# Kernel tuning notes

Hardware: AMD Instinct MI355X
Metric: run time of the kernel (lower is better)

## Reference

```python
import jax, jax.numpy as jnp
import numpy as np

N_AGENTS = 32
STATE_DIM = 6 * N_AGENTS      # 192
CONTROL_DIM = 3 * N_AGENTS    # 96
HIDDEN = 100
NEWTON_ITERS = 40

# Index maps from the cvxpy objective:
#   p[u_x_r]^T u[u_idx] + p[u_y_r]^T u[2*u_idx] + p[u_z_r]^T u[3*u_idx]
_u_idx = np.arange(N_AGENTS)
P_IDX = np.concatenate([3 * np.arange(1, N_AGENTS + 1),
                        4 * np.arange(1, N_AGENTS + 1),
                        5 * np.arange(1, N_AGENTS + 1)])
U_IDX = np.concatenate([_u_idx, 2 * _u_idx, 3 * _u_idx])


def _p_net(t, z, W1, b1, W2, b2, W3, b3):
    # DefaultPNet: MLP on concat([t, z]) with tanh hiddens (hidden_dim=100)
    x = jnp.concatenate([t, z], axis=-1)          # [B, 1+STATE_DIM]
    h = jnp.tanh(x @ W1 + b1)
    h = jnp.tanh(h @ W2 + b2)
    return h @ W3 + b3                            # [B, STATE_DIM]


def _solve_qp(q):
    # min_u q^T u + 0.5||u||^2 + 0.25||u||^4  (unconstrained, strictly convex)
    # Stationarity: q + (1+||u||^2) u = 0 => u = -q/(1+s), s = ||u||^2
    # => s (1+s)^2 = ||q||^2 ; solve scalar cubic per row via Newton.
    r = jnp.sum(q * q, axis=-1)                   # [B]
    s0 = jnp.cbrt(r)                              # good init: s ~ r^(1/3) for large r

    def step(s, _):
        one = 1.0 + s
        f = s * one * one - r
        fp = one * one + 2.0 * s * one
        return jnp.maximum(s - f / fp, 0.0), None

    s, _ = jax.lax.scan(step, s0, None, length=NEWTON_ITERS)
    return -q / (1.0 + s)[:, None]                # [B, CONTROL_DIM]


def setup_inputs() -> dict:
    key = jax.random.key(0)
    ks = jax.random.split(key, 8)
    B = 131072
    in_dim = 1 + STATE_DIM
    sc1 = 1.0 / np.sqrt(in_dim)
    sc2 = 1.0 / np.sqrt(HIDDEN)
    return {
        "z": jax.random.normal(ks[0], (B, STATE_DIM), jnp.float32),
        "t": jax.random.uniform(ks[1], (B, 1), jnp.float32),
        "W1": jax.random.normal(ks[2], (in_dim, HIDDEN), jnp.float32) * sc1,
        "b1": jnp.zeros((HIDDEN,), jnp.float32),
        "W2": jax.random.normal(ks[3], (HIDDEN, HIDDEN), jnp.float32) * sc2,
        "b2": jnp.zeros((HIDDEN,), jnp.float32),
        "W3": jax.random.normal(ks[4], (HIDDEN, STATE_DIM), jnp.float32) * sc2,
        "b3": jnp.zeros((STATE_DIM,), jnp.float32),
    }


def reference(z, t, W1, b1, W2, b2, W3, b3):
    p = _p_net(t, z, W1, b1, W2, b2, W3, b3)      # [B, STATE_DIM]
    # Accumulate linear coefficients onto u (indices overlap, so scatter-add)
    q = jnp.zeros((p.shape[0], CONTROL_DIM), p.dtype).at[:, U_IDX].add(p[:, P_IDX])
    return _solve_qp(q)                            # ustar [B, CONTROL_DIM]
```

## Files before the change

### kernel.cpp

```cpp
#include <hip/hip_runtime.h>


typedef __attribute__((ext_vector_type(8))) short short8;
typedef __attribute__((ext_vector_type(4))) float f32x4;

__device__ __forceinline__ unsigned short f2bf(float f) {
  unsigned u = __float_as_uint(f);
  u += 0x7fffu + ((u >> 16) & 1u);
  return (unsigned short)(u >> 16);
}
__device__ __forceinline__ float bf2f(unsigned short b) {
  return __uint_as_float(((unsigned)b) << 16);
}
__device__ __forceinline__ float tanh_fast(float x) {
  float ax = fabsf(x);
  float e = __builtin_amdgcn_exp2f(ax * -2.88539008177792681f);
  float r = (1.f - e) * __builtin_amdgcn_rcpf(1.f + e);
  return copysignf(r, x);
}

__global__ void cvx_prep(const float* __restrict__ W1, const float* __restrict__ b1,
                         const float* __restrict__ W2, const float* __restrict__ b2,
                         const float* __restrict__ W3, const float* __restrict__ b3,
                         short* __restrict__ pw) {
  int idx = blockIdx.x * 256 + threadIdx.x;

  if (idx < 25088) {
    int kt = idx / 3584, rem = idx % 3584;
    int nt = rem / 512, e = rem % 512;
    int lane = e >> 3, j = e & 7;
    int k = kt * 32 + (lane >> 4) * 8 + j;
    int n = nt * 16 + (lane & 15);
    float wv = 0.f;
    if (n < 100) {
      if (k < 192) wv = W1[(k + 1) * 100 + n];
      else if (k == 192) wv = W1[n];
    }
    unsigned short hi = f2bf(wv);
    unsigned short lo = f2bf(wv - bf2f(hi));
    pw[(kt * 14 + nt * 2) * 512 + e] = (short)hi;
    pw[(kt * 14 + nt * 2 + 1) * 512 + e] = (short)lo;
    return;
  }
  idx -= 25088;
  if (idx < 14336) {
    int kt = idx / 3584, rem = idx % 3584;
    int nt = rem / 512, e = rem % 512;
    int lane = e >> 3, j = e & 7;
    int k = kt * 32 + (lane >> 4) * 8 + j;
    int n = nt * 16 + (lane & 15);
    float wv = (k < 100 && n < 100) ? W2[k * 100 + n] : 0.f;
    unsigned short hi = f2bf(wv);
    unsigned short lo = f2bf(wv - bf2f(hi));
    pw[50176 + (kt * 14 + nt * 2) * 512 + e] = (short)hi;
    pw[50176 + (kt * 14 + nt * 2 + 1) * 512 + e] = (short)lo;
    return;
  }
  idx -= 14336;
  if (idx < 12288) {
    int kt = idx / 3072, rem = idx % 3072;
    int nt = rem / 512, e = rem % 512;
    int lane = e >> 3, j = e & 7;
    int k = kt * 32 + (lane >> 4) * 8 + j;
    int u = nt * 16 + (lane & 15);
    float wv = 0.f;
    if (k < 100) {
      const float* wr = W3 + k * 192;
      if (u <= 31) wv += wr[3 * u + 3];
      if ((u & 1) == 0 && u <= 62) wv += wr[2 * u + 4];
      if (u % 3 == 0 && u <= 93) wv += wr[(5 * u) / 3 + 5];
    }
    unsigned short hi = f2bf(wv);
    unsigned short lo = f2bf(wv - bf2f(hi));
    pw[78848 + (kt * 12 + nt * 2) * 512 + e] = (short)hi;
    pw[78848 + (kt * 12 + nt * 2 + 1) * 512 + e] = (short)lo;
    return;
  }
  idx -= 12288;
  float* pb = (float*)(pw + 103424);
  if (idx < 112) { pb[idx] = (idx < 100) ? b1[idx] : 0.f; return; }
  idx -= 112;
  if (idx < 112) { pb[112 + idx] = (idx < 100) ? b2[idx] : 0.f; return; }
  idx -= 112;
  if (idx < 96) {
    int u = idx;
    float v = 0.f;
    if (u <= 31) v += b3[3 * u + 3];
    if ((u & 1) == 0 && u <= 62) v += b3[2 * u + 4];
    if (u % 3 == 0 && u <= 93) v += b3[(5 * u) / 3 + 5];
    pb[224 + u] = v;
  }
}

__global__ __launch_bounds__(256, 2) void cvx_main(
    const float* __restrict__ zin, const float* __restrict__ tin,
    const short* __restrict__ pw, float* __restrict__ out) {
  __shared__ __align__(16) short wbuf[2][7168];
  __shared__ __align__(16) short hbuf[128 * 136];

  const int tid = threadIdx.x;
  const int wid = tid >> 6;
  const int lane = tid & 63;
  const int l15 = lane & 15;
  const int qd = lane >> 4;
  const int rb = blockIdx.x * 128 + wid * 32;
  const int lrb = wid * 32;

  const short* PW1 = pw;
  const short* PW2 = pw + 50176;
  const short* PW3 = pw + 78848;
  const float* pb1 = (const float*)(pw + 103424);
  const float* pb2 = pb1 + 112;
  const float* pbq = pb1 + 224;

  auto stage = [&](const short* src, int nf, int buf) {
    for (int f = wid; f < nf; f += 4) {
      const short* g = src + f * 512 + lane * 8;
      __builtin_amdgcn_global_load_lds(
          (const __attribute__((address_space(1))) void*)g,
          (__attribute__((address_space(3))) void*)&wbuf[buf][f * 512],
          16, 0, 0);
    }
  };
  stage(PW1, 14, 0);

  {
    int row = lrb + (lane >> 1);
    short8 zz = {0, 0, 0, 0, 0, 0, 0, 0};
    *(short8*)&hbuf[row * 136 + 112 + (lane & 1) * 8] = zz;
  }

  short8 XA[2][7];
#pragma unroll
  for (int mt = 0; mt < 2; mt++) {
    const int row = rb + mt * 16 + l15;
    const float* zr = zin + (size_t)row * 192;
#pragma unroll
    for (int kt = 0; kt < 6; kt++) {
      const f32x4* p0 = (const f32x4*)(zr + kt * 32 + qd * 8);
      f32x4 v0 = p0[0], v1 = p0[1];
      short8 a;
      a[0] = (short)f2bf(v0[0]); a[1] = (short)f2bf(v0[1]);
      a[2] = (short)f2bf(v0[2]); a[3] = (short)f2bf(v0[3]);
      a[4] = (short)f2bf(v1[0]); a[5] = (short)f2bf(v1[1]);
      a[6] = (short)f2bf(v1[2]); a[7] = (short)f2bf(v1[3]);
      XA[mt][kt] = a;
    }
    short8 a7 = {0, 0, 0, 0, 0, 0, 0, 0};
    if (qd == 0) a7[0] = (short)f2bf(tin[row]);
    XA[mt][6] = a7;
  }

  f32x4 acc[2][7];
#pragma unroll
  for (int nt = 0; nt < 7; nt++) {
    float bv = pb1[nt * 16 + l15];
    f32x4 bvv = {bv, bv, bv, bv};
    acc[0][nt] = bvv; acc[1][nt] = bvv;
  }
#pragma unroll
  for (int kt = 0; kt < 7; kt++) {
    __syncthreads();
    if (kt < 6) stage(PW1 + (kt + 1) * 7168, 14, (kt + 1) & 1);
    else        stage(PW2, 14, 1);
    const short* wb = wbuf[kt & 1];
#pragma unroll
    for (int nt = 0; nt < 7; nt++) {
      short8 bhi = *(const short8*)(wb + nt * 1024 + lane * 8);
      short8 blo = *(const short8*)(wb + nt * 1024 + 512 + lane * 8);
#pragma unroll
      for (int mt = 0; mt < 2; mt++) {
        acc[mt][nt] = __builtin_amdgcn_mfma_f32_16x16x32_bf16(XA[mt][kt], bhi, acc[mt][nt], 0, 0, 0);
        acc[mt][nt] = __builtin_amdgcn_mfma_f32_16x16x32_bf16(XA[mt][kt], blo, acc[mt][nt], 0, 0, 0);
      }
    }
  }
#pragma unroll
  for (int mt = 0; mt < 2; mt++)
#pragma unroll
    for (int nt = 0; nt < 7; nt++)
#pragma unroll
      for (int r = 0; r < 4; r++) {
        int row = lrb + mt * 16 + qd * 4 + r;
        hbuf[row * 136 + nt * 16 + l15] = (short)f2bf(tanh_fast(acc[mt][nt][r]));
      }

  short8 HA[2][4];
#pragma unroll
  for (int mt = 0; mt < 2; mt++) {
    int row = lrb + mt * 16 + l15;
#pragma unroll
    for (int kt = 0; kt < 4; kt++)
      HA[mt][kt] = *(const short8*)&hbuf[row * 136 + kt * 32 + qd * 8];
  }
#pragma unroll
  for (int nt = 0; nt < 7; nt++) {
    float bv = pb2[nt * 16 + l15];
    f32x4 bvv = {bv, bv, bv, bv};
    acc[0][nt] = bvv; acc[1][nt] = bvv;
  }
#pragma unroll
  for (int kt = 0; kt < 4; kt++) {
    __syncthreads();
    if (kt < 3) stage(PW2 + (kt + 1) * 7168, 14, (8 + kt) & 1);
    else        stage(PW3, 12, 1);
    const short* wb = wbuf[(7 + kt) & 1];
#pragma unroll
    for (int nt = 0; nt < 7; nt++) {
      short8 bhi = *(const short8*)(wb + nt * 1024 + lane * 8);
      short8 blo = *(const short8*)(wb + nt * 1024 + 512 + lane * 8);
#pragma unroll
      for (int mt = 0; mt < 2; mt++) {
        acc[mt][nt] = __builtin_amdgcn_mfma_f32_16x16x32_bf16(HA[mt][kt], bhi, acc[mt][nt], 0, 0, 0);
        acc[mt][nt] = __builtin_amdgcn_mfma_f32_16x16x32_bf16(HA[mt][kt], blo, acc[mt][nt], 0, 0, 0);
      }
    }
  }
#pragma unroll
  for (int mt = 0; mt < 2; mt++)
#pragma unroll
    for (int nt = 0; nt < 7; nt++)
#pragma unroll
      for (int r = 0; r < 4; r++) {
        int row = lrb + mt * 16 + qd * 4 + r;
        hbuf[row * 136 + nt * 16 + l15] = (short)f2bf(tanh_fast(acc[mt][nt][r]));
      }

#pragma unroll
  for (int mt = 0; mt < 2; mt++) {
    int row = lrb + mt * 16 + l15;
#pragma unroll
    for (int kt = 0; kt < 4; kt++)
      HA[mt][kt] = *(const short8*)&hbuf[row * 136 + kt * 32 + qd * 8];
  }
  f32x4 qacc[2][6];
#pragma unroll
  for (int nt = 0; nt < 6; nt++) {
    float bv = pbq[nt * 16 + l15];
    f32x4 bvv = {bv, bv, bv, bv};
    qacc[0][nt] = bvv; qacc[1][nt] = bvv;
  }
#pragma unroll
  for (int kt = 0; kt < 4; kt++) {
    __syncthreads();
    if (kt < 3) stage(PW3 + (kt + 1) * 6144, 12, (12 + kt) & 1);
    const short* wb = wbuf[(11 + kt) & 1];
#pragma unroll
    for (int nt = 0; nt < 6; nt++) {
      short8 bhi = *(const short8*)(wb + nt * 1024 + lane * 8);
      short8 blo = *(const short8*)(wb + nt * 1024 + 512 + lane * 8);
#pragma unroll
      for (int mt = 0; mt < 2; mt++) {
        qacc[mt][nt] = __builtin_amdgcn_mfma_f32_16x16x32_bf16(HA[mt][kt], bhi, qacc[mt][nt], 0, 0, 0);
        qacc[mt][nt] = __builtin_amdgcn_mfma_f32_16x16x32_bf16(HA[mt][kt], blo, qacc[mt][nt], 0, 0, 0);
      }
    }
  }

#pragma unroll
  for (int mt = 0; mt < 2; mt++) {
    f32x4 rs = {0.f, 0.f, 0.f, 0.f};
#pragma unroll
    for (int nt = 0; nt < 6; nt++) rs += qacc[mt][nt] * qacc[mt][nt];
    float rv[4];
#pragma unroll
    for (int r = 0; r < 4; r++) {
      float v = rs[r];
      v += __shfl_xor(v, 1);
      v += __shfl_xor(v, 2);
      v += __shfl_xor(v, 4);
      v += __shfl_xor(v, 8);
      rv[r] = v;
    }
    float r2 = rv[l15 & 3];
    float s = __builtin_amdgcn_exp2f(__builtin_amdgcn_logf(r2) * 0.333333333333f);
#pragma unroll
    for (int it = 0; it < 8; it++) {
      float one = 1.f + s;
      float fv = fmaf(s * one, one, -r2);
      float fp = one * fmaf(2.f, s, one);
      s = fmaxf(s - fv * __builtin_amdgcn_rcpf(fp), 0.f);
    }
    float myinv = -__builtin_amdgcn_rcpf(1.f + s);
#pragma unroll
    for (int r = 0; r < 4; r++) {
      float inv = __shfl(myinv, (lane & 48) | r);
      int row = rb + mt * 16 + qd * 4 + r;
      float* orow = out + (size_t)row * 96;
#pragma unroll
      for (int nt = 0; nt < 6; nt++)
        orow[nt * 16 + l15] = qacc[mt][nt][r] * inv;
    }
  }
}

extern "C" void kernel_launch(void* const* d_in, const int* in_sizes, int n_in,
                              void* d_out, int out_size, void* d_ws, size_t ws_size,
                              hipStream_t stream) {
  const float* z  = (const float*)d_in[0];
  const float* t  = (const float*)d_in[1];
  const float* W1 = (const float*)d_in[2];
  const float* b1 = (const float*)d_in[3];
  const float* W2 = (const float*)d_in[4];
  const float* b2 = (const float*)d_in[5];
  const float* W3 = (const float*)d_in[6];
  const float* b3 = (const float*)d_in[7];
  float* out = (float*)d_out;
  int B = in_sizes[0] / 192;

  short* pw = (short*)d_ws;
  cvx_prep<<<204, 256, 0, stream>>>(W1, b1, W2, b2, W3, b3, pw);
  cvx_main<<<B / 128, 256, 0, stream>>>(z, t, pw, out);
}
```

Baseline: 205.6 us.

## Drop split-bf16 weights, keep all weights resident in LDS, prefetch next rows

Weights are now stored as a single bf16 copy instead of a hi/lo pair, which halves the MFMA count and weight bytes. All three layers' weights are loaded into LDS once per 512-thread block, replacing the double-buffered per-k-tile staging and its syncs. Each block processes two 256-row chunks, with the second chunk's z loads issued early. The t input is handled as an fp32 rank-1 FMA rather than an extra K tile, and biases are added in the epilogue. The cost is lower precision in the weights and higher LDS and register use per block.

```diff
diff --git a/kernel.cpp b/kernel.cpp
--- a/kernel.cpp
+++ b/kernel.cpp
@@ -1,16 +1,17 @@
 #include <hip/hip_runtime.h>
+#include <hip/hip_bf16.h>
 
 
 typedef __attribute__((ext_vector_type(8))) short short8;
+typedef __attribute__((ext_vector_type(4))) short short4v;
 typedef __attribute__((ext_vector_type(4))) float f32x4;
+
+#define HST 116
 
 __device__ __forceinline__ unsigned short f2bf(float f) {
   unsigned u = __float_as_uint(f);
   u += 0x7fffu + ((u >> 16) & 1u);
   return (unsigned short)(u >> 16);
-}
-__device__ __forceinline__ float bf2f(unsigned short b) {
-  return __uint_as_float(((unsigned)b) << 16);
 }
 __device__ __forceinline__ float tanh_fast(float x) {
   float ax = fabsf(x);
@@ -25,24 +26,17 @@
                          short* __restrict__ pw) {
   int idx = blockIdx.x * 256 + threadIdx.x;
 
-  if (idx < 25088) {
+  if (idx < 21504) {
     int kt = idx / 3584, rem = idx % 3584;
     int nt = rem / 512, e = rem % 512;
     int lane = e >> 3, j = e & 7;
     int k = kt * 32 + (lane >> 4) * 8 + j;
     int n = nt * 16 + (lane & 15);
-    float wv = 0.f;
-    if (n < 100) {
-      if (k < 192) wv = W1[(k + 1) * 100 + n];
-      else if (k == 192) wv = W1[n];
-    }
-    unsigned short hi = f2bf(wv);
-    unsigned short lo = f2bf(wv - bf2f(hi));
-    pw[(kt * 14 + nt * 2) * 512 + e] = (short)hi;
-    pw[(kt * 14 + nt * 2 + 1) * 512 + e] = (short)lo;
+    float wv = (n < 100) ? W1[(k + 1) * 100 + n] : 0.f;
+    pw[(kt * 7 + nt) * 512 + e] = (short)f2bf(wv);
     return;
   }
-  idx -= 25088;
+  idx -= 21504;
   if (idx < 14336) {
     int kt = idx / 3584, rem = idx % 3584;
     int nt = rem / 512, e = rem % 512;
@@ -50,10 +44,7 @@
     int k = kt * 32 + (lane >> 4) * 8 + j;
     int n = nt * 16 + (lane & 15);
     float wv = (k < 100 && n < 100) ? W2[k * 100 + n] : 0.f;
-    unsigned short hi = f2bf(wv);
-    unsigned short lo = f2bf(wv - bf2f(hi));
-    pw[50176 + (kt * 14 + nt * 2) * 512 + e] = (short)hi;
-    pw[50176 + (kt * 14 + nt * 2 + 1) * 512 + e] = (short)lo;
+    pw[21504 + (kt * 7 + nt) * 512 + e] = (short)f2bf(wv);
     return;
   }
   idx -= 14336;
@@ -70,17 +61,16 @@
       if ((u & 1) == 0 && u <= 62) wv += wr[2 * u + 4];
       if (u % 3 == 0 && u <= 93) wv += wr[(5 * u) / 3 + 5];
     }
-    unsigned short hi = f2bf(wv);
-    unsigned short lo = f2bf(wv - bf2f(hi));
-    pw[78848 + (kt * 12 + nt * 2) * 512 + e] = (short)hi;
-    pw[78848 + (kt * 12 + nt * 2 + 1) * 512 + e] = (short)lo;
+    pw[35840 + (kt * 6 + nt) * 512 + e] = (short)f2bf(wv);
     return;
   }
   idx -= 12288;
-  float* pb = (float*)(pw + 103424);
-  if (idx < 112) { pb[idx] = (idx < 100) ? b1[idx] : 0.f; return; }
+  float* cb = (float*)(pw + 48128);
+  if (idx < 112) { cb[idx] = (idx < 100) ? W1[idx] : 0.f; return; }
   idx -= 112;
-  if (idx < 112) { pb[112 + idx] = (idx < 100) ? b2[idx] : 0.f; return; }
+  if (idx < 112) { cb[112 + idx] = (idx < 100) ? b1[idx] : 0.f; return; }
+  idx -= 112;
+  if (idx < 112) { cb[224 + idx] = (idx < 100) ? b2[idx] : 0.f; return; }
   idx -= 112;
   if (idx < 96) {
     int u = idx;
@@ -88,208 +78,218 @@
     if (u <= 31) v += b3[3 * u + 3];
     if ((u & 1) == 0 && u <= 62) v += b3[2 * u + 4];
     if (u % 3 == 0 && u <= 93) v += b3[(5 * u) / 3 + 5];
-    pb[224 + u] = v;
-  }
-}
-
-__global__ __launch_bounds__(256, 2) void cvx_main(
+    cb[336 + u] = v;
+  }
+}
+
+__global__ __launch_bounds__(512, 2) void cvx_main(
     const float* __restrict__ zin, const float* __restrict__ tin,
     const short* __restrict__ pw, float* __restrict__ out) {
-  __shared__ __align__(16) short wbuf[2][7168];
-  __shared__ __align__(16) short hbuf[128 * 136];
+  __shared__ __align__(16) short wbuf[48128];
+  __shared__ __align__(16) short hbuf[8 * 32 * HST];
 
   const int tid = threadIdx.x;
   const int wid = tid >> 6;
   const int lane = tid & 63;
   const int l15 = lane & 15;
   const int qd = lane >> 4;
-  const int rb = blockIdx.x * 128 + wid * 32;
-  const int lrb = wid * 32;
-
-  const short* PW1 = pw;
-  const short* PW2 = pw + 50176;
-  const short* PW3 = pw + 78848;
-  const float* pb1 = (const float*)(pw + 103424);
-  const float* pb2 = pb1 + 112;
-  const float* pbq = pb1 + 224;
-
-  auto stage = [&](const short* src, int nf, int buf) {
-    for (int f = wid; f < nf; f += 4) {
-      const short* g = src + f * 512 + lane * 8;
-      __builtin_amdgcn_global_load_lds(
-          (const __attribute__((address_space(1))) void*)g,
-          (__attribute__((address_space(3))) void*)&wbuf[buf][f * 512],
-          16, 0, 0);
-    }
+
+  for (int f = wid; f < 94; f += 8) {
+    const short* g = pw + f * 512 + lane * 8;
+    __builtin_amdgcn_global_load_lds(
+        (const __attribute__((address_space(1))) void*)g,
+        (__attribute__((address_space(3))) void*)&wbuf[f * 512], 16, 0, 0);
+  }
+
+  const float* cb = (const float*)(pw + 48128);
+  float w0v[7], b1v[7], b2v[7], bqv[6];
+#pragma unroll
+  for (int nt = 0; nt < 7; nt++) {
+    w0v[nt] = cb[nt * 16 + l15];
+    b1v[nt] = cb[112 + nt * 16 + l15];
+    b2v[nt] = cb[224 + nt * 16 + l15];
+  }
+#pragma unroll
+  for (int nt = 0; nt < 6; nt++) bqv[nt] = cb[336 + nt * 16 + l15];
+
+  const int row0 = blockIdx.x * 512 + wid * 32;
+  const int hb = wid * 32 * HST;
+
+  f32x4 zc[2][6][2];
+  float tc[2];
+#pragma unroll
+  for (int mt = 0; mt < 2; mt++) {
+    const float* zr = zin + (size_t)(row0 + mt * 16 + l15) * 192 + qd * 8;
+#pragma unroll
+    for (int kt = 0; kt < 6; kt++) {
+      zc[mt][kt][0] = *(const f32x4*)(zr + kt * 32);
+      zc[mt][kt][1] = *(const f32x4*)(zr + kt * 32 + 4);
+    }
+    tc[mt] = tin[row0 + mt * 16 + l15];
+  }
+
+  __syncthreads();
+
+  auto ldh = [&](int off) -> short8 {
+    short4v a = *(const short4v*)&hbuf[off];
+    short4v b = *(const short4v*)&hbuf[off + 4];
+    return __builtin_shufflevector(a, b, 0, 1, 2, 3, 4, 5, 6, 7);
   };
-  stage(PW1, 14, 0);
-
-  {
-    int row = lrb + (lane >> 1);
-    short8 zz = {0, 0, 0, 0, 0, 0, 0, 0};
-    *(short8*)&hbuf[row * 136 + 112 + (lane & 1) * 8] = zz;
-  }
-
-  short8 XA[2][7];
-#pragma unroll
-  for (int mt = 0; mt < 2; mt++) {
-    const int row = rb + mt * 16 + l15;
-    const float* zr = zin + (size_t)row * 192;
-#pragma unroll
-    for (int kt = 0; kt < 6; kt++) {
-      const f32x4* p0 = (const f32x4*)(zr + kt * 32 + qd * 8);
-      f32x4 v0 = p0[0], v1 = p0[1];
-      short8 a;
-      a[0] = (short)f2bf(v0[0]); a[1] = (short)f2bf(v0[1]);
-      a[2] = (short)f2bf(v0[2]); a[3] = (short)f2bf(v0[3]);
-      a[4] = (short)f2bf(v1[0]); a[5] = (short)f2bf(v1[1]);
-      a[6] = (short)f2bf(v1[2]); a[7] = (short)f2bf(v1[3]);
-      XA[mt][kt] = a;
-    }
-    short8 a7 = {0, 0, 0, 0, 0, 0, 0, 0};
-    if (qd == 0) a7[0] = (short)f2bf(tin[row]);
-    XA[mt][6] = a7;
-  }
-
-  f32x4 acc[2][7];
-#pragma unroll
-  for (int nt = 0; nt < 7; nt++) {
-    float bv = pb1[nt * 16 + l15];
-    f32x4 bvv = {bv, bv, bv, bv};
-    acc[0][nt] = bvv; acc[1][nt] = bvv;
-  }
-#pragma unroll
-  for (int kt = 0; kt < 7; kt++) {
-    __syncthreads();
-    if (kt < 6) stage(PW1 + (kt + 1) * 7168, 14, (kt + 1) & 1);
-    else        stage(PW2, 14, 1);
-    const short* wb = wbuf[kt & 1];
+
+#pragma unroll 1
+  for (int it = 0; it < 2; ++it) {
+    const int rb = row0 + it * 256;
+
+    short8 XA[2][6];
+#pragma unroll
+    for (int mt = 0; mt < 2; mt++)
+#pragma unroll
+      for (int kt = 0; kt < 6; kt++) {
+        union { short8 s; __hip_bfloat162 h[4]; } u;
+        f32x4 a = zc[mt][kt][0], b = zc[mt][kt][1];
+        u.h[0] = __float22bfloat162_rn(make_float2(a[0], a[1]));
+        u.h[1] = __float22bfloat162_rn(make_float2(a[2], a[3]));
+        u.h[2] = __float22bfloat162_rn(make_float2(b[0], b[1]));
+        u.h[3] = __float22bfloat162_rn(make_float2(b[2], b[3]));
+        XA[mt][kt] = u.s;
+      }
+    float tv0 = tc[0], tv1 = tc[1];
+
+    if (it == 0) {
+#pragma unroll
+      for (int mt = 0; mt < 2; mt++) {
+        const float* zr = zin + (size_t)(row0 + 256 + mt * 16 + l15) * 192 + qd * 8;
+#pragma unroll
+        for (int kt = 0; kt < 6; kt++) {
+          zc[mt][kt][0] = *(const f32x4*)(zr + kt * 32);
+          zc[mt][kt][1] = *(const f32x4*)(zr + kt * 32 + 4);
+        }
+        tc[mt] = tin[row0 + 256 + mt * 16 + l15];
+      }
+    }
+
+    f32x4 acc[2][7];
 #pragma unroll
     for (int nt = 0; nt < 7; nt++) {
-      short8 bhi = *(const short8*)(wb + nt * 1024 + lane * 8);
-      short8 blo = *(const short8*)(wb + nt * 1024 + 512 + lane * 8);
-#pragma unroll
-      for (int mt = 0; mt < 2; mt++) {
-        acc[mt][nt] = __builtin_amdgcn_mfma_f32_16x16x32_bf16(XA[mt][kt], bhi, acc[mt][nt], 0, 0, 0);
-        acc[mt][nt] = __builtin_amdgcn_mfma_f32_16x16x32_bf16(XA[mt][kt], blo, acc[mt][nt], 0, 0, 0);
-      }
-    }
-  }
-#pragma unroll
-  for (int mt = 0; mt < 2; mt++)
-#pragma unroll
-    for (int nt = 0; nt < 7; nt++)
+      f32x4 zzz = {0.f, 0.f, 0.f, 0.f};
+      acc[0][nt] = zzz; acc[1][nt] = zzz;
+    }
+#pragma unroll
+    for (int kt = 0; kt < 6; kt++)
+#pragma unroll
+      for (int nt = 0; nt < 7; nt++) {
+        short8 bf = *(const short8*)&wbuf[(kt * 7 + nt) * 512 + lane * 8];
+        acc[0][nt] = __builtin_amdgcn_mfma_f32_16x16x32_bf16(XA[0][kt], bf, acc[0][nt], 0, 0, 0);
+        acc[1][nt] = __builtin_amdgcn_mfma_f32_16x16x32_bf16(XA[1][kt], bf, acc[1][nt], 0, 0, 0);
+      }
+    float tr[2][4];
+#pragma unroll
+    for (int r = 0; r < 4; r++) {
+      tr[0][r] = __shfl(tv0, qd * 4 + r);
+      tr[1][r] = __shfl(tv1, qd * 4 + r);
+    }
+#pragma unroll
+    for (int mt = 0; mt < 2; mt++)
+#pragma unroll
+      for (int nt = 0; nt < 7; nt++)
+#pragma unroll
+        for (int r = 0; r < 4; r++) {
+          float v = fmaf(tr[mt][r], w0v[nt], acc[mt][nt][r] + b1v[nt]);
+          hbuf[hb + (mt * 16 + qd * 4 + r) * HST + nt * 16 + l15] = (short)f2bf(tanh_fast(v));
+        }
+
+    short8 HA[2][4];
+#pragma unroll
+    for (int mt = 0; mt < 2; mt++) {
+      int ro = hb + (mt * 16 + l15) * HST;
+#pragma unroll
+      for (int kt = 0; kt < 3; kt++) HA[mt][kt] = ldh(ro + kt * 32 + qd * 8);
+      HA[mt][3] = ldh(ro + 96 + (qd & 1) * 8);
+    }
+#pragma unroll
+    for (int nt = 0; nt < 7; nt++) {
+      f32x4 zzz = {0.f, 0.f, 0.f, 0.f};
+      acc[0][nt] = zzz; acc[1][nt] = zzz;
+    }
+#pragma unroll
+    for (int kt = 0; kt < 4; kt++)
+#pragma unroll
+      for (int nt = 0; nt < 7; nt++) {
+        short8 bf = *(const short8*)&wbuf[(42 + kt * 7 + nt) * 512 + lane * 8];
+        acc[0][nt] = __builtin_amdgcn_mfma_f32_16x16x32_bf16(HA[0][kt], bf, acc[0][nt], 0, 0, 0);
+        acc[1][nt] = __builtin_amdgcn_mfma_f32_16x16x32_bf16(HA[1][kt], bf, acc[1][nt], 0, 0, 0);
+      }
+#pragma unroll
+    for (int mt = 0; mt < 2; mt++)
+#pragma unroll
+      for (int nt = 0; nt < 7; nt++)
+#pragma unroll
+        for (int r = 0; r < 4; r++) {
+          float v = acc[mt][nt][r] + b2v[nt];
+          hbuf[hb + (mt * 16 + qd * 4 + r) * HST + nt * 16 + l15] = (short)f2bf(tanh_fast(v));
+        }
+
+#pragma unroll
+    for (int mt = 0; mt < 2; mt++) {
+      int ro = hb + (mt * 16 + l15) * HST;
+#pragma unroll
+      for (int kt = 0; kt < 3; kt++) HA[mt][kt] = ldh(ro + kt * 32 + qd * 8);
+      HA[mt][3] = ldh(ro + 96 + (qd & 1) * 8);
+    }
+    f32x4 qa[2][6];
+#pragma unroll
+    for (int nt = 0; nt < 6; nt++) {
+      f32x4 zzz = {0.f, 0.f, 0.f, 0.f};
+      qa[0][nt] = zzz; qa[1][nt] = zzz;
+    }
+#pragma unroll
+    for (int kt = 0; kt < 4; kt++)
+#pragma unroll
+      for (int nt = 0; nt < 6; nt++) {
+        short8 bf = *(const short8*)&wbuf[(70 + kt * 6 + nt) * 512 + lane * 8];
+        qa[0][nt] = __builtin_amdgcn_mfma_f32_16x16x32_bf16(HA[0][kt], bf, qa[0][nt], 0, 0, 0);
+        qa[1][nt] = __builtin_amdgcn_mfma_f32_16x16x32_bf16(HA[1][kt], bf, qa[1][nt], 0, 0, 0);
+      }
+
+#pragma unroll
+    for (int mt = 0; mt < 2; mt++) {
+#pragma unroll
+      for (int nt = 0; nt < 6; nt++) {
+        float bq = bqv[nt];
+        qa[mt][nt][0] += bq; qa[mt][nt][1] += bq;
+        qa[mt][nt][2] += bq; qa[mt][nt][3] += bq;
+      }
+      f32x4 rs = {0.f, 0.f, 0.f, 0.f};
+#pragma unroll
+      for (int nt = 0; nt < 6; nt++) rs += qa[mt][nt] * qa[mt][nt];
+      float rv[4];
 #pragma unroll
       for (int r = 0; r < 4; r++) {
-        int row = lrb + mt * 16 + qd * 4 + r;
-        hbuf[row * 136 + nt * 16 + l15] = (short)f2bf(tanh_fast(acc[mt][nt][r]));
-      }
-
-  short8 HA[2][4];
-#pragma unroll
-  for (int mt = 0; mt < 2; mt++) {
-    int row = lrb + mt * 16 + l15;
-#pragma unroll
-    for (int kt = 0; kt < 4; kt++)
-      HA[mt][kt] = *(const short8*)&hbuf[row * 136 + kt * 32 + qd * 8];
-  }
-#pragma unroll
-  for (int nt = 0; nt < 7; nt++) {
-    float bv = pb2[nt * 16 + l15];
-    f32x4 bvv = {bv, bv, bv, bv};
-    acc[0][nt] = bvv; acc[1][nt] = bvv;
-  }
-#pragma unroll
-  for (int kt = 0; kt < 4; kt++) {
-    __syncthreads();
-    if (kt < 3) stage(PW2 + (kt + 1) * 7168, 14, (8 + kt) & 1);
-    else        stage(PW3, 12, 1);
-    const short* wb = wbuf[(7 + kt) & 1];
-#pragma unroll
-    for (int nt = 0; nt < 7; nt++) {
-      short8 bhi = *(const short8*)(wb + nt * 1024 + lane * 8);
-      short8 blo = *(const short8*)(wb + nt * 1024 + 512 + lane * 8);
-#pragma unroll
-      for (int mt = 0; mt < 2; mt++) {
-        acc[mt][nt] = __builtin_amdgcn_mfma_f32_16x16x32_bf16(HA[mt][kt], bhi, acc[mt][nt], 0, 0, 0);
-        acc[mt][nt] = __builtin_amdgcn_mfma_f32_16x16x32_bf16(HA[mt][kt], blo, acc[mt][nt], 0, 0, 0);
-      }
-    }
-  }
-#pragma unroll
-  for (int mt = 0; mt < 2; mt++)
-#pragma unroll
-    for (int nt = 0; nt < 7; nt++)
+        float v = rs[r];
+        v += __shfl_xor(v, 1);
+        v += __shfl_xor(v, 2);
+        v += __shfl_xor(v, 4);
+        v += __shfl_xor(v, 8);
+        rv[r] = v;
+      }
+      float r2 = rv[l15 & 3];
+      float s = __builtin_amdgcn_exp2f(__builtin_amdgcn_logf(r2) * 0.333333333333f);
+#pragma unroll
+      for (int itn = 0; itn < 8; itn++) {
+        float one = 1.f + s;
+        float fv = fmaf(s * one, one, -r2);
+        float fp = one * fmaf(2.f, s, one);
+        s = fmaxf(s - fv * __builtin_amdgcn_rcpf(fp), 0.f);
+      }
+      float myinv = -__builtin_amdgcn_rcpf(1.f + s);
 #pragma unroll
       for (int r = 0; r < 4; r++) {
-        int row = lrb + mt * 16 + qd * 4 + r;
-        hbuf[row * 136 + nt * 16 + l15] = (short)f2bf(tanh_fast(acc[mt][nt][r]));
-      }
-
-#pragma unroll
-  for (int mt = 0; mt < 2; mt++) {
-    int row = lrb + mt * 16 + l15;
-#pragma unroll
-    for (int kt = 0; kt < 4; kt++)
-      HA[mt][kt] = *(const short8*)&hbuf[row * 136 + kt * 32 + qd * 8];
-  }
-  f32x4 qacc[2][6];
-#pragma unroll
-  for (int nt = 0; nt < 6; nt++) {
-    float bv = pbq[nt * 16 + l15];
-    f32x4 bvv = {bv, bv, bv, bv};
-    qacc[0][nt] = bvv; qacc[1][nt] = bvv;
-  }
-#pragma unroll
-  for (int kt = 0; kt < 4; kt++) {
-    __syncthreads();
-    if (kt < 3) stage(PW3 + (kt + 1) * 6144, 12, (12 + kt) & 1);
-    const short* wb = wbuf[(11 + kt) & 1];
-#pragma unroll
-    for (int nt = 0; nt < 6; nt++) {
-      short8 bhi = *(const short8*)(wb + nt * 1024 + lane * 8);
-      short8 blo = *(const short8*)(wb + nt * 1024 + 512 + lane * 8);
-#pragma unroll
-      for (int mt = 0; mt < 2; mt++) {
-        qacc[mt][nt] = __builtin_amdgcn_mfma_f32_16x16x32_bf16(HA[mt][kt], bhi, qacc[mt][nt], 0, 0, 0);
-        qacc[mt][nt] = __builtin_amdgcn_mfma_f32_16x16x32_bf16(HA[mt][kt], blo, qacc[mt][nt], 0, 0, 0);
-      }
-    }
-  }
-
-#pragma unroll
-  for (int mt = 0; mt < 2; mt++) {
-    f32x4 rs = {0.f, 0.f, 0.f, 0.f};
-#pragma unroll
-    for (int nt = 0; nt < 6; nt++) rs += qacc[mt][nt] * qacc[mt][nt];
-    float rv[4];
-#pragma unroll
-    for (int r = 0; r < 4; r++) {
-      float v = rs[r];
-      v += __shfl_xor(v, 1);
-      v += __shfl_xor(v, 2);
-      v += __shfl_xor(v, 4);
-      v += __shfl_xor(v, 8);
-      rv[r] = v;
-    }
-    float r2 = rv[l15 & 3];
-    float s = __builtin_amdgcn_exp2f(__builtin_amdgcn_logf(r2) * 0.333333333333f);
-#pragma unroll
-    for (int it = 0; it < 8; it++) {
-      float one = 1.f + s;
-      float fv = fmaf(s * one, one, -r2);
-      float fp = one * fmaf(2.f, s, one);
-      s = fmaxf(s - fv * __builtin_amdgcn_rcpf(fp), 0.f);
-    }
-    float myinv = -__builtin_amdgcn_rcpf(1.f + s);
-#pragma unroll
-    for (int r = 0; r < 4; r++) {
-      float inv = __shfl(myinv, (lane & 48) | r);
-      int row = rb + mt * 16 + qd * 4 + r;
-      float* orow = out + (size_t)row * 96;
-#pragma unroll
-      for (int nt = 0; nt < 6; nt++)
-        orow[nt * 16 + l15] = qacc[mt][nt][r] * inv;
+        float inv = __shfl(myinv, (lane & 48) | r);
+        float* orow = out + (size_t)(rb + mt * 16 + qd * 4 + r) * 96;
+#pragma unroll
+        for (int nt = 0; nt < 6; nt++)
+          orow[nt * 16 + l15] = qa[mt][nt][r] * inv;
+      }
     }
   }
 }
@@ -309,6 +309,6 @@
   int B = in_sizes[0] / 192;
 
   short* pw = (short*)d_ws;
-  cvx_prep<<<204, 256, 0, stream>>>(W1, b1, W2, b2, W3, b3, pw);
-  cvx_main<<<B / 128, 256, 0, stream>>>(z, t, pw, out);
-}
+  cvx_prep<<<190, 256, 0, stream>>>(W1, b1, W2, b2, W3, b3, pw);
+  cvx_main<<<B / 512, 512, 0, stream>>>(z, t, pw, out);
+}
```

After: 192.8 us. 6.2% less time.
